# Performance work log

Measured on AMD Instinct MI355X. Metric: run time of the kernel, lower is better.

The kernel has to match this reference:

```python
import jax, jax.numpy as jnp
import numpy as np

TEMP = 0.05
BIG = 1e6


def _mlp(z, W1, b1, W2, b2, W3, b3, W4, b4, W5, b5):
    h = jax.nn.selu(z @ W1 + b1)
    h = jax.nn.selu(h @ W2 + b2)
    h = jax.nn.selu(h @ W3 + b3)
    h = jax.nn.selu(h @ W4 + b4)
    return h @ W5 + b5


def _cdist(a, b):
    # Euclidean distance via ||a||^2 + ||b||^2 - 2 a.b (clamped for fp safety)
    d2 = (jnp.sum(a * a, axis=1)[:, None]
          + jnp.sum(b * b, axis=1)[None, :]
          - 2.0 * (a @ b.T))
    return jnp.sqrt(jnp.maximum(d2, 0.0))


def _compute_drift(x, y_pos, y_neg):
    N, N_pos = x.shape[0], y_pos.shape[0]
    dist_pos = _cdist(x, y_pos)                      # [N, N_pos]
    dist_neg = _cdist(x, y_neg)                      # [N, N_neg]
    if N == y_neg.shape[0]:
        dist_neg = dist_neg + jnp.eye(N, dtype=x.dtype) * BIG
    logit = jnp.concatenate([-dist_pos / TEMP, -dist_neg / TEMP], axis=1)
    for _ in range(5):  # Sinkhorn: alternating row / column normalization
        logit = logit - jax.nn.logsumexp(logit, axis=-1, keepdims=True)
        logit = logit - jax.nn.logsumexp(logit, axis=-2, keepdims=True)
    A = jnp.exp(logit)
    A_pos, A_neg = A[:, :N_pos], A[:, N_pos:]
    W_pos = A_pos * jnp.sum(A_neg, axis=1, keepdims=True)
    W_neg = A_neg * jnp.sum(A_pos, axis=1, keepdims=True)
    return W_pos @ y_pos - W_neg @ y_neg             # [N, D]


def _forward(pos, z, W1, b1, W2, b2, W3, b3, W4, b4, W5, b5):
    gen = _mlp(z, W1, b1, W2, b2, W3, b3, W4, b4, W5, b5)
    V = _compute_drift(gen, pos, gen)                # computed under no_grad
    target = jax.lax.stop_gradient(gen + V)
    return jnp.sum((gen - target) ** 2, axis=-1)      # per-sample loss [N]


def setup_inputs() -> dict:
    key = jax.random.key(0)
    ks = jax.random.split(key, 8)
    N, D, ND, H = 8192, 256, 128, 1024
    def w(k, fan_in, fan_out):
        return jax.random.normal(k, (fan_in, fan_out), jnp.float32) / np.float32(np.sqrt(fan_in))
    return {
        "pos": jax.random.normal(ks[0], (N, D), jnp.float32),
        "z": jax.random.normal(ks[1], (N, ND), jnp.float32),
        "W1": w(ks[2], ND, H), "b1": jnp.zeros((H,), jnp.float32),
        "W2": w(ks[3], H, H),  "b2": jnp.zeros((H,), jnp.float32),
        "W3": w(ks[4], H, H),  "b3": jnp.zeros((H,), jnp.float32),
        "W4": w(ks[5], H, H),  "b4": jnp.zeros((H,), jnp.float32),
        "W5": w(ks[6], H, D),  "b5": jnp.zeros((D,), jnp.float32),
    }


def reference(pos, z, W1, b1, W2, b2, W3, b3, W4, b4, W5, b5):
    return _forward(pos, z, W1, b1, W2, b2, W3, b3, W4, b4, W5, b5)
```

## Files before the change

kernel.cpp:

```cpp
#include <hip/hip_runtime.h>

#define DEVI __device__ __forceinline__

typedef short bf16x8 __attribute__((ext_vector_type(8)));
typedef float f32x4 __attribute__((ext_vector_type(4)));
typedef unsigned short u16;
typedef unsigned short u16x8 __attribute__((ext_vector_type(8)));
typedef unsigned short u16x4 __attribute__((ext_vector_type(4)));

enum { EPI_MLP = 0, EPI_DISTQ = 1, EPI_NEGTRI = 2 };

#define KLOG2E_T 28.853900817779268f
#define QSCALE 1846.6496523378733f
#define INVQ 0.015625f

DEVI u16 f2bf(float f) {
  unsigned u = __float_as_uint(f);
  return (u16)((u + 0x7FFFu + ((u >> 16) & 1u)) >> 16);
}
DEVI float bf2f(u16 h) { return __uint_as_float(((unsigned)h) << 16); }
DEVI float seluf(float x) {
  return x > 0.f ? 1.0507009873554805f * x : 1.7580993408473766f * expm1f(x);
}
DEVI void gload16(const void* g, void* l) {
  __builtin_amdgcn_global_load_lds(
      (const __attribute__((address_space(1))) unsigned*)g,
      (__attribute__((address_space(3))) unsigned*)l, 16, 0, 0);
}
DEVI void lse_comb(float& m, float& s, float m2, float s2) {
  float M = fmaxf(m, m2);
  s = s * exp2f(m - M) + s2 * exp2f(m2 - M);
  m = M;
}
DEVI size_t triblk(int I, int J) { return ((size_t)I * (I + 1) / 2 + J) * 4096; }

template <int R, int NW>
DEVI void stage_tile(const u16* __restrict__ src, int ld, int row0, int k0,
                     u16* lds, int wave, int lane) {
  constexpr int INST = R / (16 * NW);
#pragma unroll
  for (int t = 0; t < INST; ++t) {
    int brow = (wave * INST + t) * 16;
    int row = brow + (lane >> 2);
    int col = (lane & 3) * 8;
    gload16(src + (size_t)(row0 + row) * ld + (k0 + col), lds + brow * 32);
  }
}

template <int BM, int BN, int WM, int WN, int EPI>
__global__ __launch_bounds__(WM* WN * 64) void gemm_k(
    const u16* __restrict__ Ahi, const u16* __restrict__ Alo, int lda,
    const u16* __restrict__ Bhi, const u16* __restrict__ Blo, int ldb, int K,
    float* __restrict__ Cf, int ldc,
    const float* __restrict__ bias, int act, u16* __restrict__ Ohi,
    u16* __restrict__ Olo, int ldo,
    const float* __restrict__ xN2, const float* __restrict__ yN2,
    u16* __restrict__ Cq) {
  if constexpr (EPI == EPI_NEGTRI) {
    if (blockIdx.x > blockIdx.y) return;
  }
  constexpr int NW = WM * WN;
  constexpr int FM = BM / (WM * 16), FN = BN / (WN * 16);
  const int tid = threadIdx.x, lane = tid & 63, wave = tid >> 6;
  const int bm0 = blockIdx.y * BM, bn0 = blockIdx.x * BN;
  const int wr = (wave / WN) * (FM * 16), wc = (wave % WN) * (FN * 16);
  __shared__ __align__(16) u16 AsH[BM * 32];
  __shared__ __align__(16) u16 BsH[BN * 32];
  __shared__ __align__(16) u16 AsL[BM * 32];
  __shared__ __align__(16) u16 BsL[BN * 32];
  f32x4 acc[FM][FN] = {};
  const int fr = lane & 15, ko = (lane >> 4) * 8;
  for (int k0 = 0; k0 < K; k0 += 32) {
    stage_tile<BM, NW>(Ahi, lda, bm0, k0, AsH, wave, lane);
    stage_tile<BN, NW>(Bhi, ldb, bn0, k0, BsH, wave, lane);
    stage_tile<BM, NW>(Alo, lda, bm0, k0, AsL, wave, lane);
    stage_tile<BN, NW>(Blo, ldb, bn0, k0, BsL, wave, lane);
    __syncthreads();
    bf16x8 ah[FM], bh[FN], al[FM], bl[FN];
#pragma unroll
    for (int m = 0; m < FM; ++m) ah[m] = *(const bf16x8*)&AsH[(wr + m * 16 + fr) * 32 + ko];
#pragma unroll
    for (int n = 0; n < FN; ++n) bh[n] = *(const bf16x8*)&BsH[(wc + n * 16 + fr) * 32 + ko];
#pragma unroll
    for (int m = 0; m < FM; ++m) al[m] = *(const bf16x8*)&AsL[(wr + m * 16 + fr) * 32 + ko];
#pragma unroll
    for (int n = 0; n < FN; ++n) bl[n] = *(const bf16x8*)&BsL[(wc + n * 16 + fr) * 32 + ko];
#pragma unroll
    for (int m = 0; m < FM; ++m)
#pragma unroll
      for (int n = 0; n < FN; ++n) {
        acc[m][n] = __builtin_amdgcn_mfma_f32_16x16x32_bf16(ah[m], bh[n], acc[m][n], 0, 0, 0);
        acc[m][n] = __builtin_amdgcn_mfma_f32_16x16x32_bf16(al[m], bh[n], acc[m][n], 0, 0, 0);
        acc[m][n] = __builtin_amdgcn_mfma_f32_16x16x32_bf16(ah[m], bl[n], acc[m][n], 0, 0, 0);
      }
    __syncthreads();
  }
#pragma unroll
  for (int m = 0; m < FM; ++m)
#pragma unroll
    for (int n = 0; n < FN; ++n)
#pragma unroll
      for (int q = 0; q < 4; ++q) {
        int row = bm0 + wr + m * 16 + (lane >> 4) * 4 + q;
        int col = bn0 + wc + n * 16 + fr;
        float v = acc[m][n][q];
        if constexpr (EPI == EPI_MLP) {
          v += bias[col];
          if (act) v = seluf(v);
          u16 h = f2bf(v);
          size_t idx = (size_t)row * ldo + col;
          Ohi[idx] = h;
          Olo[idx] = f2bf(v - bf2f(h));
          if (Cf) Cf[(size_t)row * ldc + col] = v;
        } else if constexpr (EPI == EPI_DISTQ) {
          float d2 = fmaxf(xN2[row] + yN2[col] - 2.f * v, 0.f);
          float qf = fminf(QSCALE * sqrtf(d2), 65535.f);
          Cq[(size_t)row * 8192 + col] = (u16)__float2uint_rn(qf);
        } else {
          int bI = row >> 6, bJ = col >> 6;
          if (bJ <= bI) {
            float d2 = fmaxf(xN2[row] + yN2[col] - 2.f * v, 0.f);
            float qf = fminf(QSCALE * sqrtf(d2), 65535.f);
            u16 qu = (u16)__float2uint_rn(qf);
            if (row == col) qu = 65535;
            Cq[triblk(bI, bJ) + (row & 63) * 64 + (col & 63)] = qu;
          }
        }
      }
}

__global__ __launch_bounds__(256) void sink_k(
    const u16* __restrict__ DqPos, const u16* __restrict__ DqTri,
    const float* __restrict__ wpos, const float* __restrict__ wneg,
    float* __restrict__ Pm, float* __restrict__ Ps) {
  const int tid = threadIdx.x;
  const int I = blockIdx.y, q4 = blockIdx.x;
  __shared__ __align__(16) u16 stg[4096];
  __shared__ float Cm[64][12], Cs[64][12];
  const int rn = tid >> 2, cn = (tid & 3) * 16;
  const int p2 = tid & 31, g8 = tid >> 5;
  float mA = -3.0e38f, sA = 0.f;
  float mB0 = -3.0e38f, sB0 = 0.f, mB1 = -3.0e38f, sB1 = 0.f;
  const int sw = (rn & 7) << 3;

  if (DqPos) {
    const size_t rowbase = (size_t)(I * 64 + rn) * 8192;
    for (int jc = 0; jc < 32; ++jc) {
      int j0 = q4 * 2048 + jc * 64 + cn;
      u16x8 qa = *(const u16x8*)&DqPos[rowbase + j0];
      u16x8 qb = *(const u16x8*)&DqPos[rowbase + j0 + 8];
      f32x4 w0 = *(const f32x4*)&wpos[j0];
      f32x4 w1 = *(const f32x4*)&wpos[j0 + 4];
      f32x4 w2 = *(const f32x4*)&wpos[j0 + 8];
      f32x4 w3 = *(const f32x4*)&wpos[j0 + 12];
      float v[16];
#pragma unroll
      for (int e = 0; e < 4; ++e) {
        v[e] = fmaf((float)qa[e], -INVQ, -w0[e]);
        v[4 + e] = fmaf((float)qa[4 + e], -INVQ, -w1[e]);
        v[8 + e] = fmaf((float)qb[e], -INVQ, -w2[e]);
        v[12 + e] = fmaf((float)qb[4 + e], -INVQ, -w3[e]);
      }
      float mx = v[0];
#pragma unroll
      for (int e = 1; e < 16; ++e) mx = fmaxf(mx, v[e]);
      float ac = 0.f;
#pragma unroll
      for (int e = 0; e < 16; ++e) ac += exp2f(v[e] - mx);
      lse_comb(mA, sA, mx, ac);
    }
  }
  for (int Jb = q4 * 32; Jb < q4 * 32 + 32; ++Jb) {
    if (Jb <= I) {
      const u16* blk = DqTri + triblk(I, Jb);
      u16x8 qa = *(const u16x8*)&blk[rn * 64 + cn];
      u16x8 qb = *(const u16x8*)&blk[rn * 64 + cn + 8];
      int jw = Jb * 64 + cn;
      f32x4 w0 = *(const f32x4*)&wneg[jw];
      f32x4 w1 = *(const f32x4*)&wneg[jw + 4];
      f32x4 w2 = *(const f32x4*)&wneg[jw + 8];
      f32x4 w3 = *(const f32x4*)&wneg[jw + 12];
      float v[16];
#pragma unroll
      for (int e = 0; e < 4; ++e) {
        v[e] = fmaf((float)qa[e], -INVQ, -w0[e]);
        v[4 + e] = fmaf((float)qa[4 + e], -INVQ, -w1[e]);
        v[8 + e] = fmaf((float)qb[e], -INVQ, -w2[e]);
        v[12 + e] = fmaf((float)qb[4 + e], -INVQ, -w3[e]);
      }
      float mx = v[0];
#pragma unroll
      for (int e = 1; e < 16; ++e) mx = fmaxf(mx, v[e]);
      float ac = 0.f;
#pragma unroll
      for (int e = 0; e < 16; ++e) ac += exp2f(v[e] - mx);
      lse_comb(mA, sA, mx, ac);
    } else {
      const u16* blk = DqTri + triblk(Jb, I);
      u16x8 qa = *(const u16x8*)&blk[rn * 64 + cn];
      u16x8 qb = *(const u16x8*)&blk[rn * 64 + cn + 8];
      *(u16x8*)&stg[rn * 64 + (cn ^ sw)] = qa;
      *(u16x8*)&stg[rn * 64 + ((cn + 8) ^ sw)] = qb;
      __syncthreads();
      float v0[8], v1[8];
#pragma unroll
      for (int cc = 0; cc < 8; ++cc) {
        int sj = cc * 8 + g8;
        unsigned wq = *(const unsigned*)&stg[sj * 64 + ((2 * p2) ^ ((sj & 7) << 3))];
        float wgt = wneg[Jb * 64 + sj];
        v0[cc] = fmaf((float)(wq & 0xFFFFu), -INVQ, -wgt);
        v1[cc] = fmaf((float)(wq >> 16), -INVQ, -wgt);
      }
      float mx0 = v0[0], mx1 = v1[0];
#pragma unroll
      for (int cc = 1; cc < 8; ++cc) { mx0 = fmaxf(mx0, v0[cc]); mx1 = fmaxf(mx1, v1[cc]); }
      float a0 = 0.f, a1 = 0.f;
#pragma unroll
      for (int cc = 0; cc < 8; ++cc) { a0 += exp2f(v0[cc] - mx0); a1 += exp2f(v1[cc] - mx1); }
      lse_comb(mB0, sB0, mx0, a0);
      lse_comb(mB1, sB1, mx1, a1);
      __syncthreads();
    }
  }
  for (int i = tid; i < 64 * 12; i += 256) { (&Cm[0][0])[i] = -3.0e38f; (&Cs[0][0])[i] = 0.f; }
  __syncthreads();
  Cm[rn][tid & 3] = mA; Cs[rn][tid & 3] = sA;
  Cm[2 * p2][4 + g8] = mB0; Cs[2 * p2][4 + g8] = sB0;
  Cm[2 * p2 + 1][4 + g8] = mB1; Cs[2 * p2 + 1][4 + g8] = sB1;
  __syncthreads();
  if (tid < 64) {
    float m = Cm[tid][0], s = Cs[tid][0];
#pragma unroll
    for (int b = 1; b < 12; ++b) lse_comb(m, s, Cm[tid][b], Cs[tid][b]);
    Pm[(size_t)q4 * 8192 + I * 64 + tid] = m;
    Ps[(size_t)q4 * 8192 + I * 64 + tid] = s;
  }
}

__global__ void col_pos_part_k(const u16* __restrict__ Dq,
                               const float* __restrict__ rv,
                               float* __restrict__ Pm, float* __restrict__ Ps) {
  int tid = threadIdx.x;
  int j0 = blockIdx.x * 1024 + tid * 4;
  int i0 = blockIdx.y * 256;
  float m[4], s[4];
#pragma unroll
  for (int e = 0; e < 4; ++e) { m[e] = -3.0e38f; s[e] = 0.f; }
  for (int ib = 0; ib < 32; ++ib) {
    float v[4][8];
#pragma unroll
    for (int ii = 0; ii < 8; ++ii) {
      int i = i0 + ib * 8 + ii;
      u16x4 qv = *(const u16x4*)&Dq[(size_t)i * 8192 + j0];
      float ri = rv[i];
#pragma unroll
      for (int e = 0; e < 4; ++e) v[e][ii] = fmaf((float)qv[e], -INVQ, -ri);
    }
#pragma unroll
    for (int e = 0; e < 4; ++e) {
      float mx = v[e][0];
#pragma unroll
      for (int ii = 1; ii < 8; ++ii) mx = fmaxf(mx, v[e][ii]);
      float ac = 0.f;
#pragma unroll
      for (int ii = 0; ii < 8; ++ii) ac += exp2f(v[e][ii] - mx);
      lse_comb(m[e], s[e], mx, ac);
    }
  }
#pragma unroll
  for (int e = 0; e < 4; ++e) {
    Pm[(size_t)blockIdx.y * 8192 + j0 + e] = m[e];
    Ps[(size_t)blockIdx.y * 8192 + j0 + e] = s[e];
  }
}

__global__ void comb_k(const float* __restrict__ Pm, const float* __restrict__ Ps,
                       int nslots, float* __restrict__ out) {
  int j = blockIdx.x * 256 + threadIdx.x;
  float m = Pm[j], s = Ps[j];
  for (int b = 1; b < nslots; ++b)
    lse_comb(m, s, Pm[(size_t)b * 8192 + j], Ps[(size_t)b * 8192 + j]);
  out[j] = m + log2f(s);
}

template <bool NEG>
__global__ __launch_bounds__(512) void pv_k(
    const u16* __restrict__ DqPos, const u16* __restrict__ DqTri,
    const float* __restrict__ rvec, const float* __restrict__ w,
    const u16* __restrict__ BT, float* __restrict__ Mout,
    float* __restrict__ sout) {
  const int tid = threadIdx.x, lane = tid & 63, wave = tid >> 6;
  const int I = blockIdx.y;
  const int kh = blockIdx.x;
  __shared__ __align__(16) u16 AT[64 * 128];
  __shared__ __align__(16) u16 Bs[4 * 256 * 32];
  __shared__ __align__(16) u16 stg[NEG ? 2 * 4096 : 8];
  __shared__ float rvS[64];
  __shared__ float SredN[64][8];
  __shared__ float SredT[64][8];
  const int wrg = (wave >> 2) * 32, wcg = (wave & 3) * 64;
  const int fr = lane & 15, ko = (lane >> 4) * 8;
  const int rn = tid >> 3;
  const int cnp = (tid & 7) * 16;
  const int cnn = (tid & 7) * 8;
  const int swr = (rn & 7) << 3;
  const int p = tid & 63, sjg = tid >> 6;
  const int swp = (p & 7) << 3;
  float asumN = 0.f, asumT = 0.f;
  if (tid < 64) rvS[tid] = rvec[I * 64 + tid];
  __syncthreads();
  const float riN = rvS[rn];
  const float riT = rvS[p];
  f32x4 acc[2][4] = {};

  for (int jc = 0; jc < 32; ++jc) {
    const int j0 = (kh * 32 + jc) * 128;
    __syncthreads();
#pragma unroll
    for (int ks = 0; ks < 4; ++ks)
      stage_tile<256, 8>(BT, 8192, 0, j0 + ks * 32, Bs + ks * 8192, wave, lane);
    if constexpr (!NEG) {
      const u16* rp = DqPos + (size_t)(I * 64 + rn) * 8192 + j0 + cnp;
      u16x8 qa = *(const u16x8*)rp;
      u16x8 qb = *(const u16x8*)(rp + 8);
      const float* wp = w + j0 + cnp;
      f32x4 w0 = *(const f32x4*)wp;
      f32x4 w1 = *(const f32x4*)(wp + 4);
      f32x4 w2 = *(const f32x4*)(wp + 8);
      f32x4 w3 = *(const f32x4*)(wp + 12);
      union { u16x8 v; u16 e[8]; } pk0, pk1;
#pragma unroll
      for (int e = 0; e < 4; ++e) {
        float a0 = exp2f(fmaf((float)qa[e], -INVQ, -riN - w0[e]));
        float a1 = exp2f(fmaf((float)qa[4 + e], -INVQ, -riN - w1[e]));
        float a2 = exp2f(fmaf((float)qb[e], -INVQ, -riN - w2[e]));
        float a3 = exp2f(fmaf((float)qb[4 + e], -INVQ, -riN - w3[e]));
        asumN += a0 + a1 + a2 + a3;
        pk0.e[e] = f2bf(a0); pk0.e[4 + e] = f2bf(a1);
        pk1.e[e] = f2bf(a2); pk1.e[4 + e] = f2bf(a3);
      }
      *(u16x8*)&AT[rn * 128 + (cnp ^ swr)] = pk0.v;
      *(u16x8*)&AT[rn * 128 + ((cnp + 8) ^ swr)] = pk1.v;
    } else {
      bool anytr = false;
#pragma unroll
      for (int h = 0; h < 2; ++h) {
        const int Jb = kh * 64 + jc * 2 + h;
        if (Jb <= I) {
          const u16* blk = DqTri + triblk(I, Jb);
          u16x8 q = *(const u16x8*)&blk[rn * 64 + cnn];
          const float* wp = w + Jb * 64 + cnn;
          f32x4 w0 = *(const f32x4*)wp;
          f32x4 w1 = *(const f32x4*)(wp + 4);
          union { u16x8 v; u16 e[8]; } pk;
#pragma unroll
          for (int e = 0; e < 4; ++e) {
            float a0 = exp2f(fmaf((float)q[e], -INVQ, -riN - w0[e]));
            float a1 = exp2f(fmaf((float)q[4 + e], -INVQ, -riN - w1[e]));
            asumN += a0 + a1;
            pk.e[e] = f2bf(a0); pk.e[4 + e] = f2bf(a1);
          }
          *(u16x8*)&AT[rn * 128 + ((h * 64 + cnn) ^ swr)] = pk.v;
        } else {
          anytr = true;
          const u16* blk = DqTri + triblk(Jb, I);
          u16x8 q = *(const u16x8*)&blk[rn * 64 + cnn];
          *(u16x8*)&stg[h * 4096 + rn * 64 + (cnn ^ swr)] = q;
        }
      }
      if (anytr) {
        __syncthreads();
#pragma unroll
        for (int h = 0; h < 2; ++h) {
          const int Jb = kh * 64 + jc * 2 + h;
          if (Jb <= I) continue;
#pragma unroll
          for (int cc = 0; cc < 8; ++cc) {
            int sj = cc * 8 + sjg;
            u16 q = stg[h * 4096 + sj * 64 + (p ^ ((sj & 7) << 3))];
            float a = exp2f(fmaf((float)q, -INVQ, -riT - w[Jb * 64 + sj]));
            asumT += a;
            AT[p * 128 + ((h * 64 + sj) ^ swp)] = f2bf(a);
          }
        }
      }
    }
    __syncthreads();
#pragma unroll
    for (int ks = 0; ks < 4; ++ks) {
      bf16x8 a2[2], b2[4];
#pragma unroll
      for (int m = 0; m < 2; ++m) {
        int rl = wrg + m * 16 + fr;
        a2[m] = *(const bf16x8*)&AT[rl * 128 + ((ks * 32 + ko) ^ ((rl & 7) << 3))];
      }
#pragma unroll
      for (int n = 0; n < 4; ++n)
        b2[n] = *(const bf16x8*)&Bs[ks * 8192 + (wcg + n * 16 + fr) * 32 + ko];
#pragma unroll
      for (int m = 0; m < 2; ++m)
#pragma unroll
        for (int n = 0; n < 4; ++n)
          acc[m][n] = __builtin_amdgcn_mfma_f32_16x16x32_bf16(a2[m], b2[n], acc[m][n], 0, 0, 0);
    }
  }
#pragma unroll
  for (int m = 0; m < 2; ++m)
#pragma unroll
    for (int n = 0; n < 4; ++n)
#pragma unroll
      for (int q = 0; q < 4; ++q) {
        int row = I * 64 + wrg + m * 16 + (lane >> 4) * 4 + q;
        int d = wcg + n * 16 + fr;
        Mout[(size_t)kh * 2097152 + (size_t)row * 256 + d] = acc[m][n][q];
      }
  SredN[rn][tid & 7] = asumN;
  SredT[p][sjg] = NEG ? asumT : 0.f;
  __syncthreads();
  if (tid < 64) {
    float s = 0.f;
#pragma unroll
    for (int b = 0; b < 8; ++b) s += SredN[tid][b] + SredT[tid][b];
    sout[kh * 8192 + I * 64 + tid] = s;
  }
}

__global__ void convert_split_k(const float* __restrict__ src, u16* __restrict__ hi,
                                u16* __restrict__ lo, int n) {
  int i = blockIdx.x * 256 + threadIdx.x;
  if (i < n) {
    float v = src[i];
    u16 h = f2bf(v);
    hi[i] = h;
    lo[i] = f2bf(v - bf2f(h));
  }
}

__global__ void transpose_split_k(const float* __restrict__ src, int K, int N,
                                  u16* __restrict__ hi, u16* __restrict__ lo) {
  __shared__ float t[32][33];
  int x = threadIdx.x & 31, y = threadIdx.x >> 5;
  int k0 = blockIdx.x * 32, n0 = blockIdx.y * 32;
  for (int yy = y; yy < 32; yy += 8) t[yy][x] = src[(size_t)(k0 + yy) * N + n0 + x];
  __syncthreads();
  for (int yy = y; yy < 32; yy += 8) {
    float v = t[x][yy];
    size_t idx = (size_t)(n0 + yy) * K + k0 + x;
    u16 h = f2bf(v);
    hi[idx] = h;
    lo[idx] = f2bf(v - bf2f(h));
  }
}

__global__ void transpose_b16_k(const float* __restrict__ src, int M, int D,
                                u16* __restrict__ dst) {
  __shared__ float t[32][33];
  int x = threadIdx.x & 31, y = threadIdx.x >> 5;
  int m0 = blockIdx.x * 32, d0 = blockIdx.y * 32;
  for (int yy = y; yy < 32; yy += 8) t[yy][x] = src[(size_t)(m0 + yy) * D + d0 + x];
  __syncthreads();
  for (int yy = y; yy < 32; yy += 8)
    dst[(size_t)(d0 + yy) * M + m0 + x] = f2bf(t[x][yy]);
}

__global__ void rownorm_k(const float* __restrict__ src, float* __restrict__ o) {
  int i = blockIdx.x, t = threadIdx.x;
  float s = 0.f;
  for (int d = t; d < 256; d += 64) {
    float v = src[(size_t)i * 256 + d];
    s += v * v;
  }
  for (int off = 32; off; off >>= 1) s += __shfl_down(s, off, 64);
  if (t == 0) o[i] = s;
}

__global__ void zero_k(float* __restrict__ p, int n) {
  int i = blockIdx.x * 256 + threadIdx.x;
  if (i < n) p[i] = 0.f;
}

__global__ void decode_k(float* __restrict__ out, float x, int n) {
  int i = blockIdx.x * 256 + threadIdx.x;
  if (i < n) out[i] = x;
}

__global__ void final_out_k(const float* __restrict__ M1, const float* __restrict__ M2,
                            const float* __restrict__ sp, const float* __restrict__ sn,
                            float* __restrict__ out) {
  __shared__ float S[256];
  int i = blockIdx.x, d = threadIdx.x;
  size_t idx = (size_t)i * 256 + d;
  float spv = sp[i] + sp[8192 + i];
  float snv = sn[i] + sn[8192 + i];
  float v = snv * (M1[idx] + M1[2097152 + idx]) - spv * (M2[idx] + M2[2097152 + idx]);
  S[d] = v * v;
  __syncthreads();
  for (int off = 128; off; off >>= 1) {
    if (d < off) S[d] += S[d + off];
    __syncthreads();
  }
  if (d == 0) out[i] = S[0];
}

extern "C" void kernel_launch(void* const* d_in, const int* in_sizes, int n_in,
                              void* d_out, int out_size, void* d_ws, size_t ws_size,
                              hipStream_t stream) {
  (void)in_sizes; (void)n_in; (void)out_size;
  const float* pos = (const float*)d_in[0];
  const float* z   = (const float*)d_in[1];
  const float* W1  = (const float*)d_in[2];
  const float* b1  = (const float*)d_in[3];
  const float* W2  = (const float*)d_in[4];
  const float* b2  = (const float*)d_in[5];
  const float* W3  = (const float*)d_in[6];
  const float* b3  = (const float*)d_in[7];
  const float* W4  = (const float*)d_in[8];
  const float* b4  = (const float*)d_in[9];
  const float* W5  = (const float*)d_in[10];
  const float* b5  = (const float*)d_in[11];
  float* out = (float*)d_out;

  if (ws_size < (size_t)263000000) {
    decode_k<<<32, 256, 0, stream>>>(out, (float)(double)(ws_size >> 10), 8192);
    return;
  }

  char* wsp = (char*)d_ws;
  size_t off = 0;
  auto alloc = [&](size_t bytes) -> char* {
    char* p = wsp + off;
    off += (bytes + 255) & ~(size_t)255;
    return p;
  };
  u16* DqPos = (u16*)alloc((size_t)8192 * 8192 * 2);
  u16* DqTri = (u16*)alloc((size_t)8256 * 4096 * 2);
  u16* Yh    = (u16*)alloc((size_t)16384 * 256 * 2);
  u16* Yl    = (u16*)alloc((size_t)16384 * 256 * 2);
  u16* posT  = (u16*)alloc((size_t)256 * 8192 * 2);
  u16* genT  = (u16*)alloc((size_t)256 * 8192 * 2);
  float* yN2 = (float*)alloc(16384 * 4);
  float* rv  = (float*)alloc(8192 * 4);
  float* cpos = (float*)alloc(8192 * 4);
  float* cneg = (float*)alloc(8192 * 4);
  float* spv = (float*)alloc(2 * 8192 * 4);
  float* snv = (float*)alloc(2 * 8192 * 4);
  float* Pm  = (float*)alloc((size_t)32 * 8192 * 4);
  float* Ps  = (float*)alloc((size_t)32 * 8192 * 4);
  float* M1  = (float*)alloc((size_t)2 * 8192 * 256 * 4);
  float* M2  = (float*)alloc((size_t)2 * 8192 * 256 * 4);

  size_t toff = 0;
  char* tbase = (char*)DqPos;
  auto talloc = [&](size_t bytes) -> char* {
    char* p = tbase + toff;
    toff += (bytes + 255) & ~(size_t)255;
    return p;
  };
  u16* zh    = (u16*)talloc((size_t)8192 * 128 * 2);
  u16* zl    = (u16*)talloc((size_t)8192 * 128 * 2);
  u16* W1Th  = (u16*)talloc(1024 * 128 * 2);
  u16* W1Tl  = (u16*)talloc(1024 * 128 * 2);
  u16* W2Th  = (u16*)talloc(1024 * 1024 * 2);
  u16* W2Tl  = (u16*)talloc(1024 * 1024 * 2);
  u16* W3Th  = (u16*)talloc(1024 * 1024 * 2);
  u16* W3Tl  = (u16*)talloc(1024 * 1024 * 2);
  u16* W4Th  = (u16*)talloc(1024 * 1024 * 2);
  u16* W4Tl  = (u16*)talloc(1024 * 1024 * 2);
  u16* W5Th  = (u16*)talloc(256 * 1024 * 2);
  u16* W5Tl  = (u16*)talloc(256 * 1024 * 2);
  u16* h1h   = (u16*)talloc((size_t)8192 * 1024 * 2);
  u16* h1l   = (u16*)talloc((size_t)8192 * 1024 * 2);
  u16* h2h   = (u16*)talloc((size_t)8192 * 1024 * 2);
  u16* h2l   = (u16*)talloc((size_t)8192 * 1024 * 2);
  float* genf = (float*)talloc((size_t)8192 * 256 * 4);

  u16* genH = Yh + (size_t)8192 * 256;
  u16* genL = Yl + (size_t)8192 * 256;
  float* pN2 = yN2;
  float* gN2 = yN2 + 8192;

  convert_split_k<<<4096, 256, 0, stream>>>(z, zh, zl, 8192 * 128);
  convert_split_k<<<8192, 256, 0, stream>>>(pos, Yh, Yl, 8192 * 256);
  transpose_split_k<<<dim3(4, 32), 256, 0, stream>>>(W1, 128, 1024, W1Th, W1Tl);
  transpose_split_k<<<dim3(32, 32), 256, 0, stream>>>(W2, 1024, 1024, W2Th, W2Tl);
  transpose_split_k<<<dim3(32, 32), 256, 0, stream>>>(W3, 1024, 1024, W3Th, W3Tl);
  transpose_split_k<<<dim3(32, 32), 256, 0, stream>>>(W4, 1024, 1024, W4Th, W4Tl);
  transpose_split_k<<<dim3(32, 8), 256, 0, stream>>>(W5, 1024, 256, W5Th, W5Tl);
  rownorm_k<<<8192, 64, 0, stream>>>(pos, pN2);
  transpose_b16_k<<<dim3(256, 8), 256, 0, stream>>>(pos, 8192, 256, posT);

  gemm_k<128, 128, 2, 2, EPI_MLP><<<dim3(8, 64), 256, 0, stream>>>(
      zh, zl, 128, W1Th, W1Tl, 128, 128, nullptr, 0, b1, 1, h1h, h1l, 1024,
      nullptr, nullptr, nullptr);
  gemm_k<128, 128, 2, 2, EPI_MLP><<<dim3(8, 64), 256, 0, stream>>>(
      h1h, h1l, 1024, W2Th, W2Tl, 1024, 1024, nullptr, 0, b2, 1, h2h, h2l, 1024,
      nullptr, nullptr, nullptr);
  gemm_k<128, 128, 2, 2, EPI_MLP><<<dim3(8, 64), 256, 0, stream>>>(
      h2h, h2l, 1024, W3Th, W3Tl, 1024, 1024, nullptr, 0, b3, 1, h1h, h1l, 1024,
      nullptr, nullptr, nullptr);
  gemm_k<128, 128, 2, 2, EPI_MLP><<<dim3(8, 64), 256, 0, stream>>>(
      h1h, h1l, 1024, W4Th, W4Tl, 1024, 1024, nullptr, 0, b4, 1, h2h, h2l, 1024,
      nullptr, nullptr, nullptr);
  gemm_k<128, 128, 2, 2, EPI_MLP><<<dim3(2, 64), 256, 0, stream>>>(
      h2h, h2l, 1024, W5Th, W5Tl, 1024, 1024, genf, 256, b5, 0,
      genH, genL, 256, nullptr, nullptr, nullptr);

  rownorm_k<<<8192, 64, 0, stream>>>(genf, gN2);
  transpose_b16_k<<<dim3(256, 8), 256, 0, stream>>>(genf, 8192, 256, genT);

  gemm_k<128, 128, 2, 2, EPI_NEGTRI><<<dim3(64, 64), 256, 0, stream>>>(
      genH, genL, 256, genH, genL, 256, 256, nullptr, 0, nullptr, 0, nullptr,
      nullptr, 0, gN2, gN2, DqTri);
  gemm_k<128, 128, 2, 2, EPI_DISTQ><<<dim3(64, 64), 256, 0, stream>>>(
      genH, genL, 256, Yh, Yl, 256, 256, nullptr, 0, nullptr, 0, nullptr,
      nullptr, 0, gN2, pN2, DqPos);

  zero_k<<<32, 256, 0, stream>>>(cpos, 8192);
  zero_k<<<32, 256, 0, stream>>>(cneg, 8192);
  for (int it = 0; it < 5; ++it) {
    sink_k<<<dim3(4, 128), 256, 0, stream>>>(DqPos, DqTri, cpos, cneg, Pm, Ps);
    comb_k<<<32, 256, 0, stream>>>(Pm, Ps, 4, rv);
    col_pos_part_k<<<dim3(8, 32), 256, 0, stream>>>(DqPos, rv, Pm, Ps);
    comb_k<<<32, 256, 0, stream>>>(Pm, Ps, 32, cpos);
    sink_k<<<dim3(4, 128), 256, 0, stream>>>(nullptr, DqTri, nullptr, rv, Pm, Ps);
    comb_k<<<32, 256, 0, stream>>>(Pm, Ps, 4, cneg);
  }

  pv_k<false><<<dim3(2, 128), 512, 0, stream>>>(DqPos, DqTri, rv, cpos, posT, M1, spv);
  pv_k<true><<<dim3(2, 128), 512, 0, stream>>>(DqPos, DqTri, rv, cneg, genT, M2, snv);

  final_out_k<<<8192, 256, 0, stream>>>(M1, M2, spv, snv, out);
}
```

Measured before the change: 1.757 ms.

## Merge positive and negative column passes into one launch; stage GEMM epilogue stores

The column-direction Sinkhorn reductions over the positive distance matrix and over the triangular negative matrix are merged into one kernel with a combined block grid, followed by a single two-part combine kernel. This removes two launches per iteration and lets the two independent reductions share the GPU. Separately, the GEMM epilogues now write results through a swizzled shared-memory tile and emit 16-byte row-contiguous stores instead of scattered 2-byte stores. This costs extra LDS traffic and barriers, and the workspace grows for the extra partial slots.

Measured after the change: 1.783 ms. About the same (+1.4%).

```diff
diff --git a/kernel.cpp b/kernel.cpp
--- a/kernel.cpp
+++ b/kernel.cpp
@@ -64,10 +64,11 @@
   const int tid = threadIdx.x, lane = tid & 63, wave = tid >> 6;
   const int bm0 = blockIdx.y * BM, bn0 = blockIdx.x * BN;
   const int wr = (wave / WN) * (FM * 16), wc = (wave % WN) * (FN * 16);
-  __shared__ __align__(16) u16 AsH[BM * 32];
-  __shared__ __align__(16) u16 BsH[BN * 32];
-  __shared__ __align__(16) u16 AsL[BM * 32];
-  __shared__ __align__(16) u16 BsL[BN * 32];
+  __shared__ __align__(16) u16 smem[4 * BM * 32];
+  u16* AsH = smem;
+  u16* BsH = smem + BM * 32;
+  u16* AsL = smem + 2 * BM * 32;
+  u16* BsL = smem + 3 * BM * 32;
   f32x4 acc[FM][FN] = {};
   const int fr = lane & 15, ko = (lane >> 4) * 8;
   for (int k0 = 0; k0 < K; k0 += 32) {
@@ -95,38 +96,86 @@
       }
     __syncthreads();
   }
-#pragma unroll
-  for (int m = 0; m < FM; ++m)
-#pragma unroll
-    for (int n = 0; n < FN; ++n)
-#pragma unroll
-      for (int q = 0; q < 4; ++q) {
-        int row = bm0 + wr + m * 16 + (lane >> 4) * 4 + q;
-        int col = bn0 + wc + n * 16 + fr;
-        float v = acc[m][n][q];
-        if constexpr (EPI == EPI_MLP) {
-          v += bias[col];
+  const int erow = tid >> 1, ec0 = (tid & 1) * 64;
+  if constexpr (EPI == EPI_MLP) {
+#pragma unroll
+    for (int m = 0; m < FM; ++m)
+#pragma unroll
+      for (int n = 0; n < FN; ++n)
+#pragma unroll
+        for (int q = 0; q < 4; ++q) {
+          int rowl = wr + m * 16 + (lane >> 4) * 4 + q;
+          int coll = wc + n * 16 + fr;
+          float v = acc[m][n][q] + bias[bn0 + coll];
           if (act) v = seluf(v);
+          acc[m][n][q] = v;
+          if (Cf) Cf[(size_t)(bm0 + rowl) * ldc + bn0 + coll] = v;
+          smem[rowl * 128 + (coll ^ ((rowl & 7) << 3))] = f2bf(v);
+        }
+    __syncthreads();
+    {
+      u16* dst = Ohi + (size_t)(bm0 + erow) * ldo + bn0 + ec0;
+#pragma unroll
+      for (int t = 0; t < 8; ++t)
+        *(u16x8*)(dst + t * 8) =
+            *(const u16x8*)&smem[erow * 128 + ((ec0 + t * 8) ^ ((erow & 7) << 3))];
+    }
+    __syncthreads();
+#pragma unroll
+    for (int m = 0; m < FM; ++m)
+#pragma unroll
+      for (int n = 0; n < FN; ++n)
+#pragma unroll
+        for (int q = 0; q < 4; ++q) {
+          int rowl = wr + m * 16 + (lane >> 4) * 4 + q;
+          int coll = wc + n * 16 + fr;
+          float v = acc[m][n][q];
           u16 h = f2bf(v);
-          size_t idx = (size_t)row * ldo + col;
-          Ohi[idx] = h;
-          Olo[idx] = f2bf(v - bf2f(h));
-          if (Cf) Cf[(size_t)row * ldc + col] = v;
-        } else if constexpr (EPI == EPI_DISTQ) {
-          float d2 = fmaxf(xN2[row] + yN2[col] - 2.f * v, 0.f);
+          smem[rowl * 128 + (coll ^ ((rowl & 7) << 3))] = f2bf(v - bf2f(h));
+        }
+    __syncthreads();
+    {
+      u16* dst = Olo + (size_t)(bm0 + erow) * ldo + bn0 + ec0;
+#pragma unroll
+      for (int t = 0; t < 8; ++t)
+        *(u16x8*)(dst + t * 8) =
+            *(const u16x8*)&smem[erow * 128 + ((ec0 + t * 8) ^ ((erow & 7) << 3))];
+    }
+  } else {
+#pragma unroll
+    for (int m = 0; m < FM; ++m)
+#pragma unroll
+      for (int n = 0; n < FN; ++n)
+#pragma unroll
+        for (int q = 0; q < 4; ++q) {
+          int rowl = wr + m * 16 + (lane >> 4) * 4 + q;
+          int coll = wc + n * 16 + fr;
+          int grow = bm0 + rowl, gcol = bn0 + coll;
+          float d2 = fmaxf(xN2[grow] + yN2[gcol] - 2.f * acc[m][n][q], 0.f);
           float qf = fminf(QSCALE * sqrtf(d2), 65535.f);
-          Cq[(size_t)row * 8192 + col] = (u16)__float2uint_rn(qf);
-        } else {
-          int bI = row >> 6, bJ = col >> 6;
-          if (bJ <= bI) {
-            float d2 = fmaxf(xN2[row] + yN2[col] - 2.f * v, 0.f);
-            float qf = fminf(QSCALE * sqrtf(d2), 65535.f);
-            u16 qu = (u16)__float2uint_rn(qf);
-            if (row == col) qu = 65535;
-            Cq[triblk(bI, bJ) + (row & 63) * 64 + (col & 63)] = qu;
-          }
+          u16 qu = (u16)__float2uint_rn(qf);
+          if (EPI == EPI_NEGTRI && grow == gcol) qu = 65535;
+          smem[rowl * 128 + (coll ^ ((rowl & 7) << 3))] = qu;
         }
-      }
+    __syncthreads();
+    if constexpr (EPI == EPI_DISTQ) {
+      u16* dst = Cq + (size_t)(bm0 + erow) * 8192 + bn0 + ec0;
+#pragma unroll
+      for (int t = 0; t < 8; ++t)
+        *(u16x8*)(dst + t * 8) =
+            *(const u16x8*)&smem[erow * 128 + ((ec0 + t * 8) ^ ((erow & 7) << 3))];
+    } else {
+      int grow = bm0 + erow, gc = bn0 + ec0;
+      int bI = grow >> 6, bJ = gc >> 6;
+      if (bJ <= bI) {
+        u16* dst = Cq + triblk(bI, bJ) + (size_t)(grow & 63) * 64;
+#pragma unroll
+        for (int t = 0; t < 8; ++t)
+          *(u16x8*)(dst + t * 8) =
+              *(const u16x8*)&smem[erow * 128 + ((ec0 + t * 8) ^ ((erow & 7) << 3))];
+      }
+    }
+  }
 }
 
 __global__ __launch_bounds__(256) void sink_k(
@@ -143,7 +192,7 @@
   float mB0 = -3.0e38f, sB0 = 0.f, mB1 = -3.0e38f, sB1 = 0.f;
   const int sw = (rn & 7) << 3;
 
-  if (DqPos) {
+  {
     const size_t rowbase = (size_t)(I * 64 + rn) * 8192;
     for (int jc = 0; jc < 32; ++jc) {
       int j0 = q4 * 2048 + jc * 64 + cn;
@@ -237,40 +286,117 @@
   }
 }
 
-__global__ void col_pos_part_k(const u16* __restrict__ Dq,
-                               const float* __restrict__ rv,
-                               float* __restrict__ Pm, float* __restrict__ Ps) {
-  int tid = threadIdx.x;
-  int j0 = blockIdx.x * 1024 + tid * 4;
-  int i0 = blockIdx.y * 256;
-  float m[4], s[4];
-#pragma unroll
-  for (int e = 0; e < 4; ++e) { m[e] = -3.0e38f; s[e] = 0.f; }
-  for (int ib = 0; ib < 32; ++ib) {
-    float v[4][8];
-#pragma unroll
-    for (int ii = 0; ii < 8; ++ii) {
-      int i = i0 + ib * 8 + ii;
-      u16x4 qv = *(const u16x4*)&Dq[(size_t)i * 8192 + j0];
-      float ri = rv[i];
-#pragma unroll
-      for (int e = 0; e < 4; ++e) v[e][ii] = fmaf((float)qv[e], -INVQ, -ri);
+__global__ __launch_bounds__(256) void colpass_k(
+    const u16* __restrict__ DqPos, const u16* __restrict__ DqTri,
+    const float* __restrict__ rv, float* __restrict__ Pm, float* __restrict__ Ps) {
+  const int bid = blockIdx.x, tid = threadIdx.x;
+  __shared__ __align__(16) u16 stg[4096];
+  __shared__ float Cm[64][12], Cs[64][12];
+  if (bid < 256) {
+    int j0 = (bid & 7) * 1024 + tid * 4;
+    int i0 = (bid >> 3) * 256;
+    float m[4], s[4];
+#pragma unroll
+    for (int e = 0; e < 4; ++e) { m[e] = -3.0e38f; s[e] = 0.f; }
+    for (int ib = 0; ib < 32; ++ib) {
+      float v[4][8];
+#pragma unroll
+      for (int ii = 0; ii < 8; ++ii) {
+        int i = i0 + ib * 8 + ii;
+        u16x4 qv = *(const u16x4*)&DqPos[(size_t)i * 8192 + j0];
+        float ri = rv[i];
+#pragma unroll
+        for (int e = 0; e < 4; ++e) v[e][ii] = fmaf((float)qv[e], -INVQ, -ri);
+      }
+#pragma unroll
+      for (int e = 0; e < 4; ++e) {
+        float mx = v[e][0];
+#pragma unroll
+        for (int ii = 1; ii < 8; ++ii) mx = fmaxf(mx, v[e][ii]);
+        float ac = 0.f;
+#pragma unroll
+        for (int ii = 0; ii < 8; ++ii) ac += exp2f(v[e][ii] - mx);
+        lse_comb(m[e], s[e], mx, ac);
+      }
     }
 #pragma unroll
     for (int e = 0; e < 4; ++e) {
-      float mx = v[e][0];
-#pragma unroll
-      for (int ii = 1; ii < 8; ++ii) mx = fmaxf(mx, v[e][ii]);
-      float ac = 0.f;
-#pragma unroll
-      for (int ii = 0; ii < 8; ++ii) ac += exp2f(v[e][ii] - mx);
-      lse_comb(m[e], s[e], mx, ac);
-    }
-  }
-#pragma unroll
-  for (int e = 0; e < 4; ++e) {
-    Pm[(size_t)blockIdx.y * 8192 + j0 + e] = m[e];
-    Ps[(size_t)blockIdx.y * 8192 + j0 + e] = s[e];
+      Pm[(size_t)(bid >> 3) * 8192 + j0 + e] = m[e];
+      Ps[(size_t)(bid >> 3) * 8192 + j0 + e] = s[e];
+    }
+  } else {
+    const int b = bid - 256;
+    const int q4 = b & 3, I = b >> 2;
+    const int rn = tid >> 2, cn = (tid & 3) * 16;
+    const int p2 = tid & 31, g8 = tid >> 5;
+    const int sw = (rn & 7) << 3;
+    float mA = -3.0e38f, sA = 0.f;
+    float mB0 = -3.0e38f, sB0 = 0.f, mB1 = -3.0e38f, sB1 = 0.f;
+    for (int Jb = q4 * 32; Jb < q4 * 32 + 32; ++Jb) {
+      if (Jb <= I) {
+        const u16* blk = DqTri + triblk(I, Jb);
+        u16x8 qa = *(const u16x8*)&blk[rn * 64 + cn];
+        u16x8 qb = *(const u16x8*)&blk[rn * 64 + cn + 8];
+        int jw = Jb * 64 + cn;
+        f32x4 w0 = *(const f32x4*)&rv[jw];
+        f32x4 w1 = *(const f32x4*)&rv[jw + 4];
+        f32x4 w2 = *(const f32x4*)&rv[jw + 8];
+        f32x4 w3 = *(const f32x4*)&rv[jw + 12];
+        float v[16];
+#pragma unroll
+        for (int e = 0; e < 4; ++e) {
+          v[e] = fmaf((float)qa[e], -INVQ, -w0[e]);
+          v[4 + e] = fmaf((float)qa[4 + e], -INVQ, -w1[e]);
+          v[8 + e] = fmaf((float)qb[e], -INVQ, -w2[e]);
+          v[12 + e] = fmaf((float)qb[4 + e], -INVQ, -w3[e]);
+        }
+        float mx = v[0];
+#pragma unroll
+        for (int e = 1; e < 16; ++e) mx = fmaxf(mx, v[e]);
+        float ac = 0.f;
+#pragma unroll
+        for (int e = 0; e < 16; ++e) ac += exp2f(v[e] - mx);
+        lse_comb(mA, sA, mx, ac);
+      } else {
+        const u16* blk = DqTri + triblk(Jb, I);
+        u16x8 qa = *(const u16x8*)&blk[rn * 64 + cn];
+        u16x8 qb = *(const u16x8*)&blk[rn * 64 + cn + 8];
+        *(u16x8*)&stg[rn * 64 + (cn ^ sw)] = qa;
+        *(u16x8*)&stg[rn * 64 + ((cn + 8) ^ sw)] = qb;
+        __syncthreads();
+        float v0[8], v1[8];
+#pragma unroll
+        for (int cc = 0; cc < 8; ++cc) {
+          int sj = cc * 8 + g8;
+          unsigned wq = *(const unsigned*)&stg[sj * 64 + ((2 * p2) ^ ((sj & 7) << 3))];
+          float wgt = rv[Jb * 64 + sj];
+          v0[cc] = fmaf((float)(wq & 0xFFFFu), -INVQ, -wgt);
+          v1[cc] = fmaf((float)(wq >> 16), -INVQ, -wgt);
+        }
+        float mx0 = v0[0], mx1 = v1[0];
+#pragma unroll
+        for (int cc = 1; cc < 8; ++cc) { mx0 = fmaxf(mx0, v0[cc]); mx1 = fmaxf(mx1, v1[cc]); }
+        float a0 = 0.f, a1 = 0.f;
+#pragma unroll
+        for (int cc = 0; cc < 8; ++cc) { a0 += exp2f(v0[cc] - mx0); a1 += exp2f(v1[cc] - mx1); }
+        lse_comb(mB0, sB0, mx0, a0);
+        lse_comb(mB1, sB1, mx1, a1);
+        __syncthreads();
+      }
+    }
+    for (int i = tid; i < 64 * 12; i += 256) { (&Cm[0][0])[i] = -3.0e38f; (&Cs[0][0])[i] = 0.f; }
+    __syncthreads();
+    Cm[rn][tid & 3] = mA; Cs[rn][tid & 3] = sA;
+    Cm[2 * p2][4 + g8] = mB0; Cs[2 * p2][4 + g8] = sB0;
+    Cm[2 * p2 + 1][4 + g8] = mB1; Cs[2 * p2 + 1][4 + g8] = sB1;
+    __syncthreads();
+    if (tid < 64) {
+      float m = Cm[tid][0], s = Cs[tid][0];
+#pragma unroll
+      for (int b2 = 1; b2 < 12; ++b2) lse_comb(m, s, Cm[tid][b2], Cs[tid][b2]);
+      Pm[(size_t)(32 + q4) * 8192 + I * 64 + tid] = m;
+      Ps[(size_t)(32 + q4) * 8192 + I * 64 + tid] = s;
+    }
   }
 }
 
@@ -281,6 +407,23 @@
   for (int b = 1; b < nslots; ++b)
     lse_comb(m, s, Pm[(size_t)b * 8192 + j], Ps[(size_t)b * 8192 + j]);
   out[j] = m + log2f(s);
+}
+
+__global__ void comb2_k(const float* __restrict__ Pm, const float* __restrict__ Ps,
+                        float* __restrict__ cpos, float* __restrict__ cneg) {
+  int j = blockIdx.x * 256 + threadIdx.x;
+  if (j < 8192) {
+    float m = Pm[j], s = Ps[j];
+    for (int b = 1; b < 32; ++b)
+      lse_comb(m, s, Pm[(size_t)b * 8192 + j], Ps[(size_t)b * 8192 + j]);
+    cpos[j] = m + log2f(s);
+  } else {
+    int jj = j - 8192;
+    float m = Pm[(size_t)32 * 8192 + jj], s = Ps[(size_t)32 * 8192 + jj];
+    for (int b = 33; b < 36; ++b)
+      lse_comb(m, s, Pm[(size_t)b * 8192 + jj], Ps[(size_t)b * 8192 + jj]);
+    cneg[jj] = m + log2f(s);
+  }
 }
 
 template <bool NEG>
@@ -520,7 +663,7 @@
   const float* b5  = (const float*)d_in[11];
   float* out = (float*)d_out;
 
-  if (ws_size < (size_t)263000000) {
+  if (ws_size < (size_t)263300000) {
     decode_k<<<32, 256, 0, stream>>>(out, (float)(double)(ws_size >> 10), 8192);
     return;
   }
@@ -544,8 +687,8 @@
   float* cneg = (float*)alloc(8192 * 4);
   float* spv = (float*)alloc(2 * 8192 * 4);
   float* snv = (float*)alloc(2 * 8192 * 4);
-  float* Pm  = (float*)alloc((size_t)32 * 8192 * 4);
-  float* Ps  = (float*)alloc((size_t)32 * 8192 * 4);
+  float* Pm  = (float*)alloc((size_t)36 * 8192 * 4);
+  float* Ps  = (float*)alloc((size_t)36 * 8192 * 4);
   float* M1  = (float*)alloc((size_t)2 * 8192 * 256 * 4);
   float* M2  = (float*)alloc((size_t)2 * 8192 * 256 * 4);
 
@@ -620,10 +763,8 @@
   for (int it = 0; it < 5; ++it) {
     sink_k<<<dim3(4, 128), 256, 0, stream>>>(DqPos, DqTri, cpos, cneg, Pm, Ps);
     comb_k<<<32, 256, 0, stream>>>(Pm, Ps, 4, rv);
-    col_pos_part_k<<<dim3(8, 32), 256, 0, stream>>>(DqPos, rv, Pm, Ps);
-    comb_k<<<32, 256, 0, stream>>>(Pm, Ps, 32, cpos);
-    sink_k<<<dim3(4, 128), 256, 0, stream>>>(nullptr, DqTri, nullptr, rv, Pm, Ps);
-    comb_k<<<32, 256, 0, stream>>>(Pm, Ps, 4, cneg);
+    colpass_k<<<768, 256, 0, stream>>>(DqPos, DqTri, rv, Pm, Ps);
+    comb2_k<<<64, 256, 0, stream>>>(Pm, Ps, cpos, cneg);
   }
 
   pv_k<false><<<dim3(2, 128), 512, 0, stream>>>(DqPos, DqTri, rv, cpos, posT, M1, spv);
```

## Restructure Sinkhorn passes to read each triangular distance block once per pass

Applied to the files above, without the earlier changes.

The row and column Sinkhorn passes are reorganised so that each 64x64 triangular block of the symmetric negative-distance matrix is handled by its own workgroup. That workgroup produces both the row partial and the transposed column partial from a single load. The positive row and column reductions are folded into the same launches, which cuts the kernels per iteration from six to four. The many partial slots need a larger combine buffer, which is aliased onto M1, and the combine kernels now reduce over up to 128 slots each.

After: 1.832 ms. 4.3% more time.

```diff
diff --git a/kernel.cpp b/kernel.cpp
--- a/kernel.cpp
+++ b/kernel.cpp
@@ -129,120 +129,137 @@
       }
 }
 
-__global__ __launch_bounds__(256) void sink_k(
-    const u16* __restrict__ DqPos, const u16* __restrict__ DqTri,
-    const float* __restrict__ wpos, const float* __restrict__ wneg,
-    float* __restrict__ Pm, float* __restrict__ Ps) {
-  const int tid = threadIdx.x;
-  const int I = blockIdx.y, q4 = blockIdx.x;
-  __shared__ __align__(16) u16 stg[4096];
-  __shared__ float Cm[64][12], Cs[64][12];
+DEVI void lse16(const u16x8& qa, const u16x8& qb, const float* __restrict__ w,
+                float& m, float& s) {
+  f32x4 w0 = *(const f32x4*)w;
+  f32x4 w1 = *(const f32x4*)(w + 4);
+  f32x4 w2 = *(const f32x4*)(w + 8);
+  f32x4 w3 = *(const f32x4*)(w + 12);
+  float v[16];
+#pragma unroll
+  for (int e = 0; e < 4; ++e) {
+    v[e] = fmaf((float)qa[e], -INVQ, -w0[e]);
+    v[4 + e] = fmaf((float)qa[4 + e], -INVQ, -w1[e]);
+    v[8 + e] = fmaf((float)qb[e], -INVQ, -w2[e]);
+    v[12 + e] = fmaf((float)qb[4 + e], -INVQ, -w3[e]);
+  }
+  float mx = v[0];
+#pragma unroll
+  for (int e = 1; e < 16; ++e) mx = fmaxf(mx, v[e]);
+  float ac = 0.f;
+#pragma unroll
+  for (int e = 0; e < 16; ++e) ac += exp2f(v[e] - mx);
+  lse_comb(m, s, mx, ac);
+}
+
+DEVI void tri_block_pass(const u16* __restrict__ DqTri, int bid,
+                         const float* __restrict__ w, float* __restrict__ Pm,
+                         float* __restrict__ Ps, u16* stg, float (*Cm)[8],
+                         float (*Cs)[8], int tid) {
+  int a = (int)((sqrtf(8.f * (float)bid + 1.f) - 1.f) * 0.5f);
+  while ((a + 1) * (a + 2) / 2 <= bid) ++a;
+  while (a * (a + 1) / 2 > bid) --a;
+  const int b = bid - a * (a + 1) / 2;
+  const u16* blk = DqTri + (size_t)bid * 4096;
   const int rn = tid >> 2, cn = (tid & 3) * 16;
+  u16x8 qa = *(const u16x8*)&blk[rn * 64 + cn];
+  u16x8 qb = *(const u16x8*)&blk[rn * 64 + cn + 8];
+  {
+    float m = -3.0e38f, s = 0.f;
+    lse16(qa, qb, w + b * 64 + cn, m, s);
+#pragma unroll
+    for (int mask = 1; mask <= 2; mask <<= 1) {
+      float om = __shfl_xor(m, mask);
+      float os = __shfl_xor(s, mask);
+      lse_comb(m, s, om, os);
+    }
+    if ((tid & 3) == 0) {
+      Pm[(size_t)b * 8192 + a * 64 + rn] = m;
+      Ps[(size_t)b * 8192 + a * 64 + rn] = s;
+    }
+  }
+  if (a == b) return;
+  const int sw = (rn & 7) << 3;
+  *(u16x8*)&stg[rn * 64 + (cn ^ sw)] = qa;
+  *(u16x8*)&stg[rn * 64 + ((cn + 8) ^ sw)] = qb;
+  __syncthreads();
   const int p2 = tid & 31, g8 = tid >> 5;
-  float mA = -3.0e38f, sA = 0.f;
-  float mB0 = -3.0e38f, sB0 = 0.f, mB1 = -3.0e38f, sB1 = 0.f;
-  const int sw = (rn & 7) << 3;
-
-  if (DqPos) {
-    const size_t rowbase = (size_t)(I * 64 + rn) * 8192;
-    for (int jc = 0; jc < 32; ++jc) {
-      int j0 = q4 * 2048 + jc * 64 + cn;
-      u16x8 qa = *(const u16x8*)&DqPos[rowbase + j0];
-      u16x8 qb = *(const u16x8*)&DqPos[rowbase + j0 + 8];
-      f32x4 w0 = *(const f32x4*)&wpos[j0];
-      f32x4 w1 = *(const f32x4*)&wpos[j0 + 4];
-      f32x4 w2 = *(const f32x4*)&wpos[j0 + 8];
-      f32x4 w3 = *(const f32x4*)&wpos[j0 + 12];
-      float v[16];
-#pragma unroll
-      for (int e = 0; e < 4; ++e) {
-        v[e] = fmaf((float)qa[e], -INVQ, -w0[e]);
-        v[4 + e] = fmaf((float)qa[4 + e], -INVQ, -w1[e]);
-        v[8 + e] = fmaf((float)qb[e], -INVQ, -w2[e]);
-        v[12 + e] = fmaf((float)qb[4 + e], -INVQ, -w3[e]);
-      }
-      float mx = v[0];
-#pragma unroll
-      for (int e = 1; e < 16; ++e) mx = fmaxf(mx, v[e]);
-      float ac = 0.f;
-#pragma unroll
-      for (int e = 0; e < 16; ++e) ac += exp2f(v[e] - mx);
-      lse_comb(mA, sA, mx, ac);
-    }
-  }
-  for (int Jb = q4 * 32; Jb < q4 * 32 + 32; ++Jb) {
-    if (Jb <= I) {
-      const u16* blk = DqTri + triblk(I, Jb);
-      u16x8 qa = *(const u16x8*)&blk[rn * 64 + cn];
-      u16x8 qb = *(const u16x8*)&blk[rn * 64 + cn + 8];
-      int jw = Jb * 64 + cn;
-      f32x4 w0 = *(const f32x4*)&wneg[jw];
-      f32x4 w1 = *(const f32x4*)&wneg[jw + 4];
-      f32x4 w2 = *(const f32x4*)&wneg[jw + 8];
-      f32x4 w3 = *(const f32x4*)&wneg[jw + 12];
-      float v[16];
-#pragma unroll
-      for (int e = 0; e < 4; ++e) {
-        v[e] = fmaf((float)qa[e], -INVQ, -w0[e]);
-        v[4 + e] = fmaf((float)qa[4 + e], -INVQ, -w1[e]);
-        v[8 + e] = fmaf((float)qb[e], -INVQ, -w2[e]);
-        v[12 + e] = fmaf((float)qb[4 + e], -INVQ, -w3[e]);
-      }
-      float mx = v[0];
-#pragma unroll
-      for (int e = 1; e < 16; ++e) mx = fmaxf(mx, v[e]);
-      float ac = 0.f;
-#pragma unroll
-      for (int e = 0; e < 16; ++e) ac += exp2f(v[e] - mx);
-      lse_comb(mA, sA, mx, ac);
-    } else {
-      const u16* blk = DqTri + triblk(Jb, I);
-      u16x8 qa = *(const u16x8*)&blk[rn * 64 + cn];
-      u16x8 qb = *(const u16x8*)&blk[rn * 64 + cn + 8];
-      *(u16x8*)&stg[rn * 64 + (cn ^ sw)] = qa;
-      *(u16x8*)&stg[rn * 64 + ((cn + 8) ^ sw)] = qb;
-      __syncthreads();
-      float v0[8], v1[8];
-#pragma unroll
-      for (int cc = 0; cc < 8; ++cc) {
-        int sj = cc * 8 + g8;
-        unsigned wq = *(const unsigned*)&stg[sj * 64 + ((2 * p2) ^ ((sj & 7) << 3))];
-        float wgt = wneg[Jb * 64 + sj];
-        v0[cc] = fmaf((float)(wq & 0xFFFFu), -INVQ, -wgt);
-        v1[cc] = fmaf((float)(wq >> 16), -INVQ, -wgt);
-      }
-      float mx0 = v0[0], mx1 = v1[0];
-#pragma unroll
-      for (int cc = 1; cc < 8; ++cc) { mx0 = fmaxf(mx0, v0[cc]); mx1 = fmaxf(mx1, v1[cc]); }
-      float a0 = 0.f, a1 = 0.f;
-#pragma unroll
-      for (int cc = 0; cc < 8; ++cc) { a0 += exp2f(v0[cc] - mx0); a1 += exp2f(v1[cc] - mx1); }
-      lse_comb(mB0, sB0, mx0, a0);
-      lse_comb(mB1, sB1, mx1, a1);
-      __syncthreads();
-    }
-  }
-  for (int i = tid; i < 64 * 12; i += 256) { (&Cm[0][0])[i] = -3.0e38f; (&Cs[0][0])[i] = 0.f; }
-  __syncthreads();
-  Cm[rn][tid & 3] = mA; Cs[rn][tid & 3] = sA;
-  Cm[2 * p2][4 + g8] = mB0; Cs[2 * p2][4 + g8] = sB0;
-  Cm[2 * p2 + 1][4 + g8] = mB1; Cs[2 * p2 + 1][4 + g8] = sB1;
+  float v0[8], v1[8];
+#pragma unroll
+  for (int cc = 0; cc < 8; ++cc) {
+    int sj = cc * 8 + g8;
+    unsigned wq = *(const unsigned*)&stg[sj * 64 + ((2 * p2) ^ ((sj & 7) << 3))];
+    float wgt = w[a * 64 + sj];
+    v0[cc] = fmaf((float)(wq & 0xFFFFu), -INVQ, -wgt);
+    v1[cc] = fmaf((float)(wq >> 16), -INVQ, -wgt);
+  }
+  float mx0 = v0[0], mx1 = v1[0];
+#pragma unroll
+  for (int cc = 1; cc < 8; ++cc) { mx0 = fmaxf(mx0, v0[cc]); mx1 = fmaxf(mx1, v1[cc]); }
+  float a0 = 0.f, a1 = 0.f;
+#pragma unroll
+  for (int cc = 0; cc < 8; ++cc) { a0 += exp2f(v0[cc] - mx0); a1 += exp2f(v1[cc] - mx1); }
+  Cm[2 * p2][g8] = mx0; Cs[2 * p2][g8] = a0;
+  Cm[2 * p2 + 1][g8] = mx1; Cs[2 * p2 + 1][g8] = a1;
   __syncthreads();
   if (tid < 64) {
     float m = Cm[tid][0], s = Cs[tid][0];
 #pragma unroll
-    for (int b = 1; b < 12; ++b) lse_comb(m, s, Cm[tid][b], Cs[tid][b]);
-    Pm[(size_t)q4 * 8192 + I * 64 + tid] = m;
-    Ps[(size_t)q4 * 8192 + I * 64 + tid] = s;
-  }
-}
-
-__global__ void col_pos_part_k(const u16* __restrict__ Dq,
-                               const float* __restrict__ rv,
-                               float* __restrict__ Pm, float* __restrict__ Ps) {
-  int tid = threadIdx.x;
-  int j0 = blockIdx.x * 1024 + tid * 4;
-  int i0 = blockIdx.y * 256;
+    for (int g = 1; g < 8; ++g) lse_comb(m, s, Cm[tid][g], Cs[tid][g]);
+    Pm[(size_t)a * 8192 + b * 64 + tid] = m;
+    Ps[(size_t)a * 8192 + b * 64 + tid] = s;
+  }
+}
+
+__global__ __launch_bounds__(256) void rowpass_k(
+    const u16* __restrict__ DqPos, const u16* __restrict__ DqTri,
+    const float* __restrict__ cpos, const float* __restrict__ cneg,
+    float* __restrict__ Pm, float* __restrict__ Ps) {
+  __shared__ __align__(16) u16 stg[4096];
+  __shared__ float Cm[64][8], Cs[64][8];
+  const int tid = threadIdx.x;
+  const int bid = blockIdx.x;
+  if (bid < 8256) {
+    tri_block_pass(DqTri, bid, cneg, Pm, Ps, stg, Cm, Cs, tid);
+    return;
+  }
+  const int b2 = bid - 8256;
+  const int I = b2 >> 2, q4 = b2 & 3;
+  const int rn = tid >> 2, cn = (tid & 3) * 16;
+  const size_t rowbase = (size_t)(I * 64 + rn) * 8192;
+  float m = -3.0e38f, s = 0.f;
+  for (int jc = 0; jc < 32; ++jc) {
+    int j0 = q4 * 2048 + jc * 64 + cn;
+    u16x8 qa = *(const u16x8*)&DqPos[rowbase + j0];
+    u16x8 qb = *(const u16x8*)&DqPos[rowbase + j0 + 8];
+    lse16(qa, qb, cpos + j0, m, s);
+  }
+#pragma unroll
+  for (int mask = 1; mask <= 2; mask <<= 1) {
+    float om = __shfl_xor(m, mask);
+    float os = __shfl_xor(s, mask);
+    lse_comb(m, s, om, os);
+  }
+  if ((tid & 3) == 0) {
+    Pm[(size_t)(128 + q4) * 8192 + I * 64 + rn] = m;
+    Ps[(size_t)(128 + q4) * 8192 + I * 64 + rn] = s;
+  }
+}
+
+__global__ __launch_bounds__(256) void colpass2_k(
+    const u16* __restrict__ DqPos, const u16* __restrict__ DqTri,
+    const float* __restrict__ rv, float* __restrict__ Pm, float* __restrict__ Ps) {
+  __shared__ __align__(16) u16 stg[4096];
+  __shared__ float Cm[64][8], Cs[64][8];
+  const int tid = threadIdx.x;
+  const int bid = blockIdx.x;
+  if (bid < 8256) {
+    tri_block_pass(DqTri, bid, rv, Pm, Ps, stg, Cm, Cs, tid);
+    return;
+  }
+  const int b2 = bid - 8256;
+  int j0 = (b2 & 7) * 1024 + tid * 4;
+  int i0 = (b2 >> 3) * 256;
   float m[4], s[4];
 #pragma unroll
   for (int e = 0; e < 4; ++e) { m[e] = -3.0e38f; s[e] = 0.f; }
@@ -251,7 +268,7 @@
 #pragma unroll
     for (int ii = 0; ii < 8; ++ii) {
       int i = i0 + ib * 8 + ii;
-      u16x4 qv = *(const u16x4*)&Dq[(size_t)i * 8192 + j0];
+      u16x4 qv = *(const u16x4*)&DqPos[(size_t)i * 8192 + j0];
       float ri = rv[i];
 #pragma unroll
       for (int e = 0; e < 4; ++e) v[e][ii] = fmaf((float)qv[e], -INVQ, -ri);
@@ -269,18 +286,35 @@
   }
 #pragma unroll
   for (int e = 0; e < 4; ++e) {
-    Pm[(size_t)blockIdx.y * 8192 + j0 + e] = m[e];
-    Ps[(size_t)blockIdx.y * 8192 + j0 + e] = s[e];
-  }
-}
-
-__global__ void comb_k(const float* __restrict__ Pm, const float* __restrict__ Ps,
-                       int nslots, float* __restrict__ out) {
+    Pm[(size_t)(128 + (b2 >> 3)) * 8192 + j0 + e] = m[e];
+    Ps[(size_t)(128 + (b2 >> 3)) * 8192 + j0 + e] = s[e];
+  }
+}
+
+__global__ void comb_rv_k(const float* __restrict__ Pm, const float* __restrict__ Ps,
+                          float* __restrict__ rv) {
   int j = blockIdx.x * 256 + threadIdx.x;
   float m = Pm[j], s = Ps[j];
-  for (int b = 1; b < nslots; ++b)
+  for (int b = 1; b < 132; ++b)
     lse_comb(m, s, Pm[(size_t)b * 8192 + j], Ps[(size_t)b * 8192 + j]);
-  out[j] = m + log2f(s);
+  rv[j] = m + log2f(s);
+}
+
+__global__ void comb_cpc_k(const float* __restrict__ Pm, const float* __restrict__ Ps,
+                           float* __restrict__ cpos, float* __restrict__ cneg) {
+  int j = blockIdx.x * 256 + threadIdx.x;
+  if (j < 8192) {
+    float m = Pm[(size_t)128 * 8192 + j], s = Ps[(size_t)128 * 8192 + j];
+    for (int b = 129; b < 160; ++b)
+      lse_comb(m, s, Pm[(size_t)b * 8192 + j], Ps[(size_t)b * 8192 + j]);
+    cpos[j] = m + log2f(s);
+  } else {
+    int jj = j - 8192;
+    float m = Pm[jj], s = Ps[jj];
+    for (int b = 1; b < 128; ++b)
+      lse_comb(m, s, Pm[(size_t)b * 8192 + jj], Ps[(size_t)b * 8192 + jj]);
+    cneg[jj] = m + log2f(s);
+  }
 }
 
 template <bool NEG>
@@ -520,7 +554,7 @@
   const float* b5  = (const float*)d_in[11];
   float* out = (float*)d_out;
 
-  if (ws_size < (size_t)263000000) {
+  if (ws_size < (size_t)261500000) {
     decode_k<<<32, 256, 0, stream>>>(out, (float)(double)(ws_size >> 10), 8192);
     return;
   }
@@ -544,10 +578,10 @@
   float* cneg = (float*)alloc(8192 * 4);
   float* spv = (float*)alloc(2 * 8192 * 4);
   float* snv = (float*)alloc(2 * 8192 * 4);
-  float* Pm  = (float*)alloc((size_t)32 * 8192 * 4);
-  float* Ps  = (float*)alloc((size_t)32 * 8192 * 4);
   float* M1  = (float*)alloc((size_t)2 * 8192 * 256 * 4);
   float* M2  = (float*)alloc((size_t)2 * 8192 * 256 * 4);
+  float* Pm = M1;
+  float* Ps = (float*)((char*)M1 + (size_t)160 * 8192 * 4);
 
   size_t toff = 0;
   char* tbase = (char*)DqPos;
@@ -615,15 +649,12 @@
       genH, genL, 256, Yh, Yl, 256, 256, nullptr, 0, nullptr, 0, nullptr,
       nullptr, 0, gN2, pN2, DqPos);
 
-  zero_k<<<32, 256, 0, stream>>>(cpos, 8192);
-  zero_k<<<32, 256, 0, stream>>>(cneg, 8192);
+  zero_k<<<64, 256, 0, stream>>>(cpos, 16384);
   for (int it = 0; it < 5; ++it) {
-    sink_k<<<dim3(4, 128), 256, 0, stream>>>(DqPos, DqTri, cpos, cneg, Pm, Ps);
-    comb_k<<<32, 256, 0, stream>>>(Pm, Ps, 4, rv);
-    col_pos_part_k<<<dim3(8, 32), 256, 0, stream>>>(DqPos, rv, Pm, Ps);
-    comb_k<<<32, 256, 0, stream>>>(Pm, Ps, 32, cpos);
-    sink_k<<<dim3(4, 128), 256, 0, stream>>>(nullptr, DqTri, nullptr, rv, Pm, Ps);
-    comb_k<<<32, 256, 0, stream>>>(Pm, Ps, 4, cneg);
+    rowpass_k<<<8768, 256, 0, stream>>>(DqPos, DqTri, cpos, cneg, Pm, Ps);
+    comb_rv_k<<<32, 256, 0, stream>>>(Pm, Ps, rv);
+    colpass2_k<<<8512, 256, 0, stream>>>(DqPos, DqTri, rv, Pm, Ps);
+    comb_cpc_k<<<64, 256, 0, stream>>>(Pm, Ps, cpos, cneg);
   }
 
   pv_k<false><<<dim3(2, 128), 512, 0, stream>>>(DqPos, DqTri, rv, cpos, posT, M1, spv);
```
